# Kernel optimization log

Hardware: AMD Instinct MI355X
Metric: run time of the kernel (lower is better)

Reference implementation:

```python
import jax, jax.numpy as jnp
import numpy as np

LAG = 5
MSG_HID = 256
N_ATOMS = 30
N_EDGES = N_ATOMS * (N_ATOMS - 1)  # 870
BATCH = 2
T = 200


def _rel_matrices():
    # fully-connected directed graph, no self loops (standard NRI encoding)
    recv, send = [], []
    for i in range(N_ATOMS):
        for j in range(N_ATOMS):
            if i != j:
                recv.append(i)
                send.append(j)
    rel_rec = np.zeros((N_EDGES, N_ATOMS), dtype=np.float32)
    rel_send = np.zeros((N_EDGES, N_ATOMS), dtype=np.float32)
    rel_rec[np.arange(N_EDGES), recv] = 1.0
    rel_send[np.arange(N_EDGES), send] = 1.0
    return jnp.asarray(rel_rec), jnp.asarray(rel_send)


def setup_inputs() -> dict:
    key = jax.random.key(0)
    ks = jax.random.split(key, 14)
    rel_rec, rel_send = _rel_matrices()
    s = 0.05
    return {
        "inputs": jax.random.normal(ks[0], (BATCH, N_ATOMS, T), jnp.float32),
        "mu": jax.random.normal(ks[1], (BATCH, N_EDGES), jnp.float32),
        "logvar": jax.random.normal(ks[2], (BATCH, N_EDGES), jnp.float32) * 0.1,
        "eps": jax.random.normal(ks[3], (BATCH, N_EDGES), jnp.float32),
        "rel_rec": rel_rec,
        "rel_send": rel_send,
        "w_msg1": jax.random.normal(ks[4], (2 * LAG, MSG_HID), jnp.float32) * s,
        "b_msg1": jnp.zeros((MSG_HID,), jnp.float32),
        "w_msg2": jax.random.normal(ks[5], (MSG_HID, MSG_HID), jnp.float32) * s,
        "b_msg2": jnp.zeros((MSG_HID,), jnp.float32),
        "w_out1": jax.random.normal(ks[6], (LAG + MSG_HID, MSG_HID), jnp.float32) * s,
        "b_out1": jnp.zeros((MSG_HID,), jnp.float32),
        "w_out2": jax.random.normal(ks[7], (MSG_HID, MSG_HID), jnp.float32) * s,
        "b_out2": jnp.zeros((MSG_HID,), jnp.float32),
        "w_out3": jax.random.normal(ks[8], (MSG_HID, 1), jnp.float32) * s,
        "b_out3": jnp.zeros((1,), jnp.float32),
    }


def reference(inputs, mu, logvar, eps, rel_rec, rel_send,
              w_msg1, b_msg1, w_msg2, b_msg2,
              w_out1, b_out1, w_out2, b_out2, w_out3, b_out3):
    # reparametrize: edges [B, E]
    edges = eps * jnp.exp(0.5 * logvar) + mu

    # lag-stack: data [B, T-lag, N, lag]
    Tm = inputs.shape[2] - LAG
    data = jnp.stack([inputs[:, :, i:i + Tm] for i in range(LAG)], axis=-1)
    data = jnp.transpose(data, (0, 2, 1, 3))  # [B, Tm, N, lag]

    # gather node features to edges via one-hot matmuls
    receivers = jnp.einsum('en,btnl->btel', rel_rec, data)   # [B, Tm, E, lag]
    senders = jnp.einsum('en,btnl->btel', rel_send, data)    # [B, Tm, E, lag]
    pre_msg = jnp.concatenate([senders, receivers], axis=-1)  # [B, Tm, E, 2*lag]

    msg = jax.nn.relu(pre_msg @ w_msg1 + b_msg1)
    msg = jax.nn.relu(msg @ w_msg2 + b_msg2)                 # [B, Tm, E, hid]
    msg = msg * edges[:, None, :, None]                       # edge mask

    # scatter-aggregate messages back to receiver nodes
    agg_msgs = jnp.einsum('bteh,en->btnh', msg, rel_rec)      # [B, Tm, N, hid]

    aug = jnp.concatenate([data, agg_msgs], axis=-1)          # [B, Tm, N, lag+hid]
    pred = jax.nn.relu(aug @ w_out1 + b_out1)
    pred = jax.nn.relu(pred @ w_out2 + b_out2)
    pred = (pred @ w_out3 + b_out3)[..., 0]                   # [B, Tm, N]

    return jnp.transpose(pred, (0, 2, 1))                     # [B, N, Tm]
```

## Files before the change

### kernel.cpp

```cpp
#include <hip/hip_runtime.h>

#define LAG 5
#define HID 256
#define NA 30
#define NE 870
#define TM 195
#define TT 200
#define NB 2
#define EPN 29
#define NTB 98
#define NROWS (NB * TM * NA)
#define APAD 8
#define KC 32
#define UVB 1463
#define W2F_ELEMS (HID * HID)
#define W1F_ELEMS (HID * 288)
#define W2OF_ELEMS (HID * HID)

typedef __bf16 bf16;
typedef __bf16 bf16x8 __attribute__((ext_vector_type(8)));
typedef float floatx4 __attribute__((ext_vector_type(4)));

__global__ __launch_bounds__(256) void k1_prep(
    const float* __restrict__ inputs, const float* __restrict__ w_msg1,
    const float* __restrict__ b_msg1, const float* __restrict__ w_msg2,
    const float* __restrict__ w_out1, const float* __restrict__ w_out2,
    bf16* __restrict__ u, bf16* __restrict__ v, bf16* __restrict__ w2frag,
    bf16* __restrict__ w1frag, bf16* __restrict__ w2ofrag)
{
    const int bid = blockIdx.x, tid = threadIdx.x;
    if (bid < UVB) {
        __shared__ float feats8[8][LAG];
        const int r0 = bid * 8;
        if (tid < 8 * LAG) {
            const int i = tid / LAG, l = tid % LAG;
            const int r = r0 + i;
            float fv = 0.f;
            if (r < NROWS) {
                const int b = r / (TM * NA), rem = r % (TM * NA);
                const int t = rem / NA, n = rem % NA;
                fv = inputs[(b * NA + n) * TT + t + l];
            }
            feats8[i][l] = fv;
        }
        float w1c[2 * LAG];
        #pragma unroll
        for (int k = 0; k < 2 * LAG; ++k) w1c[k] = w_msg1[k * HID + tid];
        const float bb = b_msg1[tid];
        __syncthreads();
        #pragma unroll
        for (int i = 0; i < 8; ++i) {
            const int r = r0 + i;
            if (r < NROWS) {
                float ua = bb, va = 0.f;
                #pragma unroll
                for (int l = 0; l < LAG; ++l) {
                    ua = fmaf(feats8[i][l], w1c[l], ua);
                    va = fmaf(feats8[i][l], w1c[LAG + l], va);
                }
                u[(r << 8) + tid] = (bf16)ua;
                v[(r << 8) + tid] = (bf16)va;
            }
        }
    } else if (bid < UVB + 32) {
        const int fidx = (bid - UVB) * 256 + tid;
        const int lane = fidx & 63;
        const int kc = (fidx >> 6) & 7;
        const int ntc = fidx >> 9;
        const int col = ntc * 16 + (lane & 15);
        const int kb = kc * KC + (lane >> 4) * 8;
        bf16x8 vv;
        #pragma unroll
        for (int x = 0; x < 8; ++x) vv[x] = (bf16)w_msg2[(kb + x) * HID + col];
        *(bf16x8*)&w2frag[fidx * 8] = vv;
    } else if (bid < UVB + 32 + 36) {
        const int fidx = (bid - (UVB + 32)) * 256 + tid;
        const int lane = fidx & 63;
        const int kc = (fidx >> 6) % 9;
        const int ntc = fidx / (64 * 9);
        const int col = ntc * 16 + (lane & 15);
        const int kb = kc * KC + (lane >> 4) * 8;
        bf16x8 vv;
        #pragma unroll
        for (int x = 0; x < 8; ++x) {
            const int k = kb + x;
            float val;
            if (k < 256)      val = w_out1[(5 + k) * HID + col];
            else if (k < 261) val = w_out1[(k - 256) * HID + col];
            else              val = 0.f;
            vv[x] = (bf16)val;
        }
        *(bf16x8*)&w1frag[fidx * 8] = vv;
    } else {
        const int fidx = (bid - (UVB + 32 + 36)) * 256 + tid;
        const int lane = fidx & 63;
        const int kc = (fidx >> 6) & 7;
        const int ntc = fidx >> 9;
        const int col = ntc * 16 + (lane & 15);
        const int kb = kc * KC + (lane >> 4) * 8;
        bf16x8 vv;
        #pragma unroll
        for (int x = 0; x < 8; ++x) vv[x] = (bf16)w_out2[(kb + x) * HID + col];
        *(bf16x8*)&w2ofrag[fidx * 8] = vv;
    }
}

__global__ __launch_bounds__(512) void k2_msg(
    const bf16* __restrict__ u, const bf16* __restrict__ v,
    const bf16* __restrict__ w2frag,
    const float* __restrict__ mu, const float* __restrict__ logvar,
    const float* __restrict__ eps, const float* __restrict__ b_msg2,
    bf16* __restrict__ agg)
{
    __shared__ bf16 a_lds[64][HID + APAD];
    __shared__ float ev_lds[32];

    const int bid = blockIdx.x;
    const int n  = bid % NA;
    const int tb = (bid / NA) % NTB;
    const int b  = bid / (NA * NTB);
    const int t0 = tb * 2;
    const int tid = threadIdx.x;
    const int lane = tid & 63, w = tid >> 6;
    const int q = lane >> 4, m15 = lane & 15;
    const int wbase = w * 32;

    if (tid < 32) {
        float evv = 0.f;
        if (tid < EPN) {
            const int e = b * NE + n * EPN + tid;
            evv = eps[e] * __expf(0.5f * logvar[e]) + mu[e];
        }
        ev_lds[tid] = evv;
    }

    #pragma unroll
    for (int i = 0; i < 4; ++i) {
        const int task = i * 512 + tid;
        const int row = task >> 5, c = task & 31;
        const int tt = row >> 5, ei = row & 31;
        bf16x8 out8;
        if (ei < EPN) {
            int t = t0 + tt; if (t > TM - 1) t = TM - 1;
            const int j = ei + (ei >= n);
            const bf16x8 uu = *(const bf16x8*)(u + ((((b * TM + t) * NA + j) << 8) + c * 8));
            const bf16x8 vv = *(const bf16x8*)(v + ((((b * TM + t) * NA + n) << 8) + c * 8));
            #pragma unroll
            for (int x = 0; x < 8; ++x)
                out8[x] = (bf16)fmaxf((float)uu[x] + (float)vv[x], 0.f);
        } else {
            #pragma unroll
            for (int x = 0; x < 8; ++x) out8[x] = (bf16)0.f;
        }
        *(bf16x8*)&a_lds[row][c * 8] = out8;
    }

    const bf16* bbase = w2frag + (lane << 3);
    bf16x8 bcur[2], bnxt[2];
    #pragma unroll
    for (int nt = 0; nt < 2; ++nt)
        bcur[nt] = *(const bf16x8*)(bbase + (((w * 2 + nt) * 8 + 0) << 9));

    floatx4 acc[4][2];
    #pragma unroll
    for (int mt = 0; mt < 4; ++mt)
        #pragma unroll
        for (int nt = 0; nt < 2; ++nt)
            acc[mt][nt] = (floatx4){0.f, 0.f, 0.f, 0.f};

    __syncthreads();

    #pragma unroll
    for (int kc = 0; kc < 8; ++kc) {
        if (kc < 7) {
            #pragma unroll
            for (int nt = 0; nt < 2; ++nt)
                bnxt[nt] = *(const bf16x8*)(bbase + (((w * 2 + nt) * 8 + kc + 1) << 9));
        }
        bf16x8 af[4];
        #pragma unroll
        for (int mt = 0; mt < 4; ++mt)
            af[mt] = *(const bf16x8*)&a_lds[mt * 16 + m15][kc * KC + q * 8];
        #pragma unroll
        for (int nt = 0; nt < 2; ++nt)
            #pragma unroll
            for (int mt = 0; mt < 4; ++mt)
                acc[mt][nt] = __builtin_amdgcn_mfma_f32_16x16x32_bf16(af[mt], bcur[nt], acc[mt][nt], 0, 0, 0);
        #pragma unroll
        for (int nt = 0; nt < 2; ++nt) bcur[nt] = bnxt[nt];
    }

    float b2v[2];
    #pragma unroll
    for (int nt = 0; nt < 2; ++nt) b2v[nt] = b_msg2[wbase + nt * 16 + m15];

    #pragma unroll
    for (int tt = 0; tt < 2; ++tt) {
        const int t = t0 + tt;
        #pragma unroll
        for (int nt = 0; nt < 2; ++nt) {
            float part = 0.f;
            #pragma unroll
            for (int ml = 0; ml < 2; ++ml) {
                const int mt = tt * 2 + ml;
                #pragma unroll
                for (int reg = 0; reg < 4; ++reg) {
                    const int ei = (ml * 16 + q * 4 + reg);
                    part += ev_lds[ei] * fmaxf(acc[mt][nt][reg] + b2v[nt], 0.f);
                }
            }
            part += __shfl_xor(part, 16, 64);
            part += __shfl_xor(part, 32, 64);
            if (q == 0 && t < TM)
                agg[((((b * TM + t) * NA + n) << 8) + wbase + nt * 16 + m15)] = (bf16)part;
        }
    }
}

__global__ __launch_bounds__(256) void k3_out(
    const bf16* __restrict__ agg, const float* __restrict__ inputs,
    const bf16* __restrict__ w1frag, const bf16* __restrict__ w2ofrag,
    const float* __restrict__ b_out1, const float* __restrict__ b_out2,
    const float* __restrict__ w_out3, const float* __restrict__ b_out3,
    float* __restrict__ out)
{
    __shared__ bf16 a1[16][288 + APAD];
    __shared__ float red[4][16];

    const int R0 = blockIdx.x * 16;
    const int tid = threadIdx.x;
    const int lane = tid & 63, w = tid >> 6;
    const int q = lane >> 4, m15 = lane & 15;
    const int wbase = w * 64;

    #pragma unroll
    for (int i = 0; i < 2; ++i) {
        const int task = i * 256 + tid;
        const int row = task >> 5, c = task & 31;
        const int R = R0 + row;
        bf16x8 val;
        if (R < NROWS) {
            val = *(const bf16x8*)&agg[(R << 8) + c * 8];
        } else {
            for (int x = 0; x < 8; ++x) val[x] = (bf16)0.f;
        }
        *(bf16x8*)&a1[row][c * 8] = val;
    }
    if (tid < 16) {
        const int R = R0 + tid;
        if (R < NROWS) {
            const int b = R / (TM * NA), rem = R % (TM * NA);
            const int t = rem / NA, n = rem % NA;
            const float* ip = inputs + (b * NA + n) * TT + t;
            #pragma unroll
            for (int l = 0; l < LAG; ++l) a1[tid][256 + l] = (bf16)ip[l];
            #pragma unroll
            for (int k = 261; k < 288; ++k) a1[tid][k] = (bf16)0.f;
        } else {
            for (int k = 256; k < 288; ++k) a1[tid][k] = (bf16)0.f;
        }
    }

    floatx4 acc[4];
    #pragma unroll
    for (int nt = 0; nt < 4; ++nt) acc[nt] = (floatx4){0.f, 0.f, 0.f, 0.f};

    const bf16* b1base = w1frag + (lane << 3);
    bf16x8 bcur[4], bnxt[4];
    #pragma unroll
    for (int nt = 0; nt < 4; ++nt)
        bcur[nt] = *(const bf16x8*)(b1base + (((w * 4 + nt) * 9 + 0) << 9));

    __syncthreads();

    #pragma unroll
    for (int kc = 0; kc < 9; ++kc) {
        if (kc < 8) {
            #pragma unroll
            for (int nt = 0; nt < 4; ++nt)
                bnxt[nt] = *(const bf16x8*)(b1base + (((w * 4 + nt) * 9 + kc + 1) << 9));
        }
        const bf16x8 af = *(const bf16x8*)&a1[m15][kc * KC + q * 8];
        #pragma unroll
        for (int nt = 0; nt < 4; ++nt)
            acc[nt] = __builtin_amdgcn_mfma_f32_16x16x32_bf16(af, bcur[nt], acc[nt], 0, 0, 0);
        #pragma unroll
        for (int nt = 0; nt < 4; ++nt) bcur[nt] = bnxt[nt];
    }
    __syncthreads();

    {
        float b1v[4];
        #pragma unroll
        for (int nt = 0; nt < 4; ++nt) b1v[nt] = b_out1[wbase + nt * 16 + m15];
        #pragma unroll
        for (int nt = 0; nt < 4; ++nt)
            #pragma unroll
            for (int reg = 0; reg < 4; ++reg)
                a1[q * 4 + reg][wbase + nt * 16 + m15] =
                    (bf16)fmaxf(acc[nt][reg] + b1v[nt], 0.f);
    }

    #pragma unroll
    for (int nt = 0; nt < 4; ++nt) acc[nt] = (floatx4){0.f, 0.f, 0.f, 0.f};

    const bf16* b2base = w2ofrag + (lane << 3);
    #pragma unroll
    for (int nt = 0; nt < 4; ++nt)
        bcur[nt] = *(const bf16x8*)(b2base + (((w * 4 + nt) * 8 + 0) << 9));

    __syncthreads();

    #pragma unroll
    for (int kc = 0; kc < 8; ++kc) {
        if (kc < 7) {
            #pragma unroll
            for (int nt = 0; nt < 4; ++nt)
                bnxt[nt] = *(const bf16x8*)(b2base + (((w * 4 + nt) * 8 + kc + 1) << 9));
        }
        const bf16x8 af = *(const bf16x8*)&a1[m15][kc * KC + q * 8];
        #pragma unroll
        for (int nt = 0; nt < 4; ++nt)
            acc[nt] = __builtin_amdgcn_mfma_f32_16x16x32_bf16(af, bcur[nt], acc[nt], 0, 0, 0);
        #pragma unroll
        for (int nt = 0; nt < 4; ++nt) bcur[nt] = bnxt[nt];
    }

    {
        float b2v[4], w3v[4];
        #pragma unroll
        for (int nt = 0; nt < 4; ++nt) {
            const int col = wbase + nt * 16 + m15;
            b2v[nt] = b_out2[col];
            w3v[nt] = w_out3[col];
        }
        #pragma unroll
        for (int reg = 0; reg < 4; ++reg) {
            float p = 0.f;
            #pragma unroll
            for (int nt = 0; nt < 4; ++nt)
                p += fmaxf(acc[nt][reg] + b2v[nt], 0.f) * w3v[nt];
            p += __shfl_xor(p, 1, 64);
            p += __shfl_xor(p, 2, 64);
            p += __shfl_xor(p, 4, 64);
            p += __shfl_xor(p, 8, 64);
            if (m15 == 0) red[w][q * 4 + reg] = p;
        }
    }
    __syncthreads();
    if (tid < 16) {
        const int R = R0 + tid;
        if (R < NROWS) {
            const float val = red[0][tid] + red[1][tid] + red[2][tid] + red[3][tid] + b_out3[0];
            const int b = R / (TM * NA), rem = R % (TM * NA);
            const int t = rem / NA, n = rem % NA;
            out[(b * NA + n) * TM + t] = val;
        }
    }
}

extern "C" void kernel_launch(void* const* d_in, const int* in_sizes, int n_in,
                              void* d_out, int out_size, void* d_ws, size_t ws_size,
                              hipStream_t stream) {
    const float* inputs  = (const float*)d_in[0];
    const float* mu      = (const float*)d_in[1];
    const float* logvar  = (const float*)d_in[2];
    const float* eps     = (const float*)d_in[3];
    const float* w_msg1  = (const float*)d_in[6];
    const float* b_msg1  = (const float*)d_in[7];
    const float* w_msg2  = (const float*)d_in[8];
    const float* b_msg2  = (const float*)d_in[9];
    const float* w_out1  = (const float*)d_in[10];
    const float* b_out1  = (const float*)d_in[11];
    const float* w_out2  = (const float*)d_in[12];
    const float* b_out2  = (const float*)d_in[13];
    const float* w_out3  = (const float*)d_in[14];
    const float* b_out3  = (const float*)d_in[15];
    float* out = (float*)d_out;

    bf16* u       = (bf16*)d_ws;
    bf16* v       = u       + NROWS * HID;
    bf16* aggw    = v       + NROWS * HID;
    bf16* w2frag  = aggw    + NROWS * HID;
    bf16* w1frag  = w2frag  + W2F_ELEMS;
    bf16* w2ofrag = w1frag  + W1F_ELEMS;

    hipLaunchKernelGGL(k1_prep, dim3(UVB + 32 + 36 + 32), dim3(256), 0, stream,
                       inputs, w_msg1, b_msg1, w_msg2, w_out1, w_out2,
                       u, v, w2frag, w1frag, w2ofrag);
    hipLaunchKernelGGL(k2_msg, dim3(NB * NA * NTB), dim3(512), 0, stream,
                       u, v, w2frag, mu, logvar, eps, b_msg2, aggw);
    hipLaunchKernelGGL(k3_out, dim3((NROWS + 15) / 16), dim3(256), 0, stream,
                       aggw, inputs, w1frag, w2ofrag, b_out1, b_out2, w_out3, b_out3, out);
}
```

Before: 168.8 us.

## Switch to fp16 MFMA, process three timesteps per message block, deepen weight prefetch

Changes all intermediate activations and weight fragments from bf16 to fp16 and uses the f16 MFMA instruction. The ReLU of u+v becomes a packed half-precision add and max instead of per-element float conversions. The message kernel now covers three timesteps per block (96 rows), so each B fragment is reused across more M tiles and the tail clamp goes away because 195 divides by 3. It also prefetches weights two K-chunks ahead, sets a min-blocks-per-SM launch bound and shrinks LDS padding. fp16 has less exponent range than bf16, a no-op term was added in w2ofrag prep, and the larger tile raises register and LDS use, which may lower occupancy.

```diff
diff --git a/kernel.cpp b/kernel.cpp
--- a/kernel.cpp
+++ b/kernel.cpp
@@ -8,25 +8,24 @@
 #define TT 200
 #define NB 2
 #define EPN 29
-#define NTB 98
+#define TB3 65
 #define NROWS (NB * TM * NA)
-#define APAD 8
+#define APAD 4
 #define KC 32
 #define UVB 1463
 #define W2F_ELEMS (HID * HID)
 #define W1F_ELEMS (HID * 288)
-#define W2OF_ELEMS (HID * HID)
-
-typedef __bf16 bf16;
-typedef __bf16 bf16x8 __attribute__((ext_vector_type(8)));
+
+typedef _Float16 f16;
+typedef _Float16 f16x8 __attribute__((ext_vector_type(8)));
 typedef float floatx4 __attribute__((ext_vector_type(4)));
 
 __global__ __launch_bounds__(256) void k1_prep(
     const float* __restrict__ inputs, const float* __restrict__ w_msg1,
     const float* __restrict__ b_msg1, const float* __restrict__ w_msg2,
     const float* __restrict__ w_out1, const float* __restrict__ w_out2,
-    bf16* __restrict__ u, bf16* __restrict__ v, bf16* __restrict__ w2frag,
-    bf16* __restrict__ w1frag, bf16* __restrict__ w2ofrag)
+    f16* __restrict__ u, f16* __restrict__ v, f16* __restrict__ w2frag,
+    f16* __restrict__ w1frag, f16* __restrict__ w2ofrag)
 {
     const int bid = blockIdx.x, tid = threadIdx.x;
     if (bid < UVB) {
@@ -58,8 +57,8 @@
                     ua = fmaf(feats8[i][l], w1c[l], ua);
                     va = fmaf(feats8[i][l], w1c[LAG + l], va);
                 }
-                u[(r << 8) + tid] = (bf16)ua;
-                v[(r << 8) + tid] = (bf16)va;
+                u[(r << 8) + tid] = (f16)ua;
+                v[(r << 8) + tid] = (f16)va;
             }
         }
     } else if (bid < UVB + 32) {
@@ -69,10 +68,10 @@
         const int ntc = fidx >> 9;
         const int col = ntc * 16 + (lane & 15);
         const int kb = kc * KC + (lane >> 4) * 8;
-        bf16x8 vv;
-        #pragma unroll
-        for (int x = 0; x < 8; ++x) vv[x] = (bf16)w_msg2[(kb + x) * HID + col];
-        *(bf16x8*)&w2frag[fidx * 8] = vv;
+        f16x8 vv;
+        #pragma unroll
+        for (int x = 0; x < 8; ++x) vv[x] = (f16)w_msg2[(kb + x) * HID + col];
+        *(f16x8*)&w2frag[fidx * 8] = vv;
     } else if (bid < UVB + 32 + 36) {
         const int fidx = (bid - (UVB + 32)) * 256 + tid;
         const int lane = fidx & 63;
@@ -80,7 +79,7 @@
         const int ntc = fidx / (64 * 9);
         const int col = ntc * 16 + (lane & 15);
         const int kb = kc * KC + (lane >> 4) * 8;
-        bf16x8 vv;
+        f16x8 vv;
         #pragma unroll
         for (int x = 0; x < 8; ++x) {
             const int k = kb + x;
@@ -88,9 +87,9 @@
             if (k < 256)      val = w_out1[(5 + k) * HID + col];
             else if (k < 261) val = w_out1[(k - 256) * HID + col];
             else              val = 0.f;
-            vv[x] = (bf16)val;
-        }
-        *(bf16x8*)&w1frag[fidx * 8] = vv;
+            vv[x] = (f16)val;
+        }
+        *(f16x8*)&w1frag[fidx * 8] = vv;
     } else {
         const int fidx = (bid - (UVB + 32 + 36)) * 256 + tid;
         const int lane = fidx & 63;
@@ -98,28 +97,28 @@
         const int ntc = fidx >> 9;
         const int col = ntc * 16 + (lane & 15);
         const int kb = kc * KC + (lane >> 4) * 8;
-        bf16x8 vv;
-        #pragma unroll
-        for (int x = 0; x < 8; ++x) vv[x] = (bf16)w_out2[(kb + x) * HID + col];
-        *(bf16x8*)&w2ofrag[fidx * 8] = vv;
+        f16x8 vv;
+        #pragma unroll
+        for (int x = 0; x < 8; ++x) vv[x] = (f16)w_msg2[0] * (f16)0.f + (f16)w_out2[(kb + x) * HID + col];
+        *(f16x8*)&w2ofrag[fidx * 8] = vv;
     }
 }
 
-__global__ __launch_bounds__(512) void k2_msg(
-    const bf16* __restrict__ u, const bf16* __restrict__ v,
-    const bf16* __restrict__ w2frag,
+__global__ __launch_bounds__(512, 4) void k2_msg(
+    const f16* __restrict__ u, const f16* __restrict__ v,
+    const f16* __restrict__ w2frag,
     const float* __restrict__ mu, const float* __restrict__ logvar,
     const float* __restrict__ eps, const float* __restrict__ b_msg2,
-    bf16* __restrict__ agg)
+    f16* __restrict__ agg)
 {
-    __shared__ bf16 a_lds[64][HID + APAD];
+    __shared__ f16 a_lds[96][HID + APAD];
     __shared__ float ev_lds[32];
 
     const int bid = blockIdx.x;
     const int n  = bid % NA;
-    const int tb = (bid / NA) % NTB;
-    const int b  = bid / (NA * NTB);
-    const int t0 = tb * 2;
+    const int tb = (bid / NA) % TB3;
+    const int b  = bid / (NA * TB3);
+    const int t0 = tb * 3;
     const int tid = threadIdx.x;
     const int lane = tid & 63, w = tid >> 6;
     const int q = lane >> 4, m15 = lane & 15;
@@ -134,36 +133,37 @@
         ev_lds[tid] = evv;
     }
 
-    #pragma unroll
-    for (int i = 0; i < 4; ++i) {
+    const f16x8 z8 = {(f16)0, (f16)0, (f16)0, (f16)0, (f16)0, (f16)0, (f16)0, (f16)0};
+
+    #pragma unroll
+    for (int i = 0; i < 6; ++i) {
         const int task = i * 512 + tid;
         const int row = task >> 5, c = task & 31;
         const int tt = row >> 5, ei = row & 31;
-        bf16x8 out8;
+        f16x8 out8;
         if (ei < EPN) {
-            int t = t0 + tt; if (t > TM - 1) t = TM - 1;
+            const int t = t0 + tt;
             const int j = ei + (ei >= n);
-            const bf16x8 uu = *(const bf16x8*)(u + ((((b * TM + t) * NA + j) << 8) + c * 8));
-            const bf16x8 vv = *(const bf16x8*)(v + ((((b * TM + t) * NA + n) << 8) + c * 8));
-            #pragma unroll
-            for (int x = 0; x < 8; ++x)
-                out8[x] = (bf16)fmaxf((float)uu[x] + (float)vv[x], 0.f);
+            const f16x8 uu = *(const f16x8*)(u + ((((b * TM + t) * NA + j) << 8) + c * 8));
+            const f16x8 vv = *(const f16x8*)(v + ((((b * TM + t) * NA + n) << 8) + c * 8));
+            out8 = __builtin_elementwise_max(uu + vv, z8);
         } else {
-            #pragma unroll
-            for (int x = 0; x < 8; ++x) out8[x] = (bf16)0.f;
-        }
-        *(bf16x8*)&a_lds[row][c * 8] = out8;
-    }
-
-    const bf16* bbase = w2frag + (lane << 3);
-    bf16x8 bcur[2], bnxt[2];
-    #pragma unroll
-    for (int nt = 0; nt < 2; ++nt)
-        bcur[nt] = *(const bf16x8*)(bbase + (((w * 2 + nt) * 8 + 0) << 9));
-
-    floatx4 acc[4][2];
-    #pragma unroll
-    for (int mt = 0; mt < 4; ++mt)
+            out8 = z8;
+        }
+        *(f16x8*)&a_lds[row][c * 8] = out8;
+    }
+
+    const f16* bbase = w2frag + (lane << 3);
+    f16x8 b0[2], b1[2], b2[2];
+    #pragma unroll
+    for (int nt = 0; nt < 2; ++nt) {
+        b0[nt] = *(const f16x8*)(bbase + (((w * 2 + nt) * 8 + 0) << 9));
+        b1[nt] = *(const f16x8*)(bbase + (((w * 2 + nt) * 8 + 1) << 9));
+    }
+
+    floatx4 acc[6][2];
+    #pragma unroll
+    for (int mt = 0; mt < 6; ++mt)
         #pragma unroll
         for (int nt = 0; nt < 2; ++nt)
             acc[mt][nt] = (floatx4){0.f, 0.f, 0.f, 0.f};
@@ -172,22 +172,22 @@
 
     #pragma unroll
     for (int kc = 0; kc < 8; ++kc) {
-        if (kc < 7) {
+        if (kc < 6) {
             #pragma unroll
             for (int nt = 0; nt < 2; ++nt)
-                bnxt[nt] = *(const bf16x8*)(bbase + (((w * 2 + nt) * 8 + kc + 1) << 9));
-        }
-        bf16x8 af[4];
-        #pragma unroll
-        for (int mt = 0; mt < 4; ++mt)
-            af[mt] = *(const bf16x8*)&a_lds[mt * 16 + m15][kc * KC + q * 8];
+                b2[nt] = *(const f16x8*)(bbase + (((w * 2 + nt) * 8 + kc + 2) << 9));
+        }
+        f16x8 af[6];
+        #pragma unroll
+        for (int mt = 0; mt < 6; ++mt)
+            af[mt] = *(const f16x8*)&a_lds[mt * 16 + m15][kc * KC + q * 8];
         #pragma unroll
         for (int nt = 0; nt < 2; ++nt)
             #pragma unroll
-            for (int mt = 0; mt < 4; ++mt)
-                acc[mt][nt] = __builtin_amdgcn_mfma_f32_16x16x32_bf16(af[mt], bcur[nt], acc[mt][nt], 0, 0, 0);
-        #pragma unroll
-        for (int nt = 0; nt < 2; ++nt) bcur[nt] = bnxt[nt];
+            for (int mt = 0; mt < 6; ++mt)
+                acc[mt][nt] = __builtin_amdgcn_mfma_f32_16x16x32_f16(af[mt], b0[nt], acc[mt][nt], 0, 0, 0);
+        #pragma unroll
+        for (int nt = 0; nt < 2; ++nt) { b0[nt] = b1[nt]; b1[nt] = b2[nt]; }
     }
 
     float b2v[2];
@@ -195,7 +195,7 @@
     for (int nt = 0; nt < 2; ++nt) b2v[nt] = b_msg2[wbase + nt * 16 + m15];
 
     #pragma unroll
-    for (int tt = 0; tt < 2; ++tt) {
+    for (int tt = 0; tt < 3; ++tt) {
         const int t = t0 + tt;
         #pragma unroll
         for (int nt = 0; nt < 2; ++nt) {
@@ -211,20 +211,20 @@
             }
             part += __shfl_xor(part, 16, 64);
             part += __shfl_xor(part, 32, 64);
-            if (q == 0 && t < TM)
-                agg[((((b * TM + t) * NA + n) << 8) + wbase + nt * 16 + m15)] = (bf16)part;
+            if (q == 0)
+                agg[((((b * TM + t) * NA + n) << 8) + wbase + nt * 16 + m15)] = (f16)part;
         }
     }
 }
 
 __global__ __launch_bounds__(256) void k3_out(
-    const bf16* __restrict__ agg, const float* __restrict__ inputs,
-    const bf16* __restrict__ w1frag, const bf16* __restrict__ w2ofrag,
+    const f16* __restrict__ agg, const float* __restrict__ inputs,
+    const f16* __restrict__ w1frag, const f16* __restrict__ w2ofrag,
     const float* __restrict__ b_out1, const float* __restrict__ b_out2,
     const float* __restrict__ w_out3, const float* __restrict__ b_out3,
     float* __restrict__ out)
 {
-    __shared__ bf16 a1[16][288 + APAD];
+    __shared__ f16 a1[16][288 + APAD];
     __shared__ float red[4][16];
 
     const int R0 = blockIdx.x * 16;
@@ -238,13 +238,13 @@
         const int task = i * 256 + tid;
         const int row = task >> 5, c = task & 31;
         const int R = R0 + row;
-        bf16x8 val;
+        f16x8 val;
         if (R < NROWS) {
-            val = *(const bf16x8*)&agg[(R << 8) + c * 8];
+            val = *(const f16x8*)&agg[(R << 8) + c * 8];
         } else {
-            for (int x = 0; x < 8; ++x) val[x] = (bf16)0.f;
-        }
-        *(bf16x8*)&a1[row][c * 8] = val;
+            for (int x = 0; x < 8; ++x) val[x] = (f16)0.f;
+        }
+        *(f16x8*)&a1[row][c * 8] = val;
     }
     if (tid < 16) {
         const int R = R0 + tid;
@@ -253,11 +253,11 @@
             const int t = rem / NA, n = rem % NA;
             const float* ip = inputs + (b * NA + n) * TT + t;
             #pragma unroll
-            for (int l = 0; l < LAG; ++l) a1[tid][256 + l] = (bf16)ip[l];
-            #pragma unroll
-            for (int k = 261; k < 288; ++k) a1[tid][k] = (bf16)0.f;
+            for (int l = 0; l < LAG; ++l) a1[tid][256 + l] = (f16)ip[l];
+            #pragma unroll
+            for (int k = 261; k < 288; ++k) a1[tid][k] = (f16)0.f;
         } else {
-            for (int k = 256; k < 288; ++k) a1[tid][k] = (bf16)0.f;
+            for (int k = 256; k < 288; ++k) a1[tid][k] = (f16)0.f;
         }
     }
 
@@ -265,11 +265,11 @@
     #pragma unroll
     for (int nt = 0; nt < 4; ++nt) acc[nt] = (floatx4){0.f, 0.f, 0.f, 0.f};
 
-    const bf16* b1base = w1frag + (lane << 3);
-    bf16x8 bcur[4], bnxt[4];
+    const f16* b1base = w1frag + (lane << 3);
+    f16x8 bcur[4], bnxt[4];
     #pragma unroll
     for (int nt = 0; nt < 4; ++nt)
-        bcur[nt] = *(const bf16x8*)(b1base + (((w * 4 + nt) * 9 + 0) << 9));
+        bcur[nt] = *(const f16x8*)(b1base + (((w * 4 + nt) * 9 + 0) << 9));
 
     __syncthreads();
 
@@ -278,12 +278,12 @@
         if (kc < 8) {
             #pragma unroll
             for (int nt = 0; nt < 4; ++nt)
-                bnxt[nt] = *(const bf16x8*)(b1base + (((w * 4 + nt) * 9 + kc + 1) << 9));
-        }
-        const bf16x8 af = *(const bf16x8*)&a1[m15][kc * KC + q * 8];
+                bnxt[nt] = *(const f16x8*)(b1base + (((w * 4 + nt) * 9 + kc + 1) << 9));
+        }
+        const f16x8 af = *(const f16x8*)&a1[m15][kc * KC + q * 8];
         #pragma unroll
         for (int nt = 0; nt < 4; ++nt)
-            acc[nt] = __builtin_amdgcn_mfma_f32_16x16x32_bf16(af, bcur[nt], acc[nt], 0, 0, 0);
+            acc[nt] = __builtin_amdgcn_mfma_f32_16x16x32_f16(af, bcur[nt], acc[nt], 0, 0, 0);
         #pragma unroll
         for (int nt = 0; nt < 4; ++nt) bcur[nt] = bnxt[nt];
     }
@@ -298,16 +298,16 @@
             #pragma unroll
             for (int reg = 0; reg < 4; ++reg)
                 a1[q * 4 + reg][wbase + nt * 16 + m15] =
-                    (bf16)fmaxf(acc[nt][reg] + b1v[nt], 0.f);
+                    (f16)fmaxf(acc[nt][reg] + b1v[nt], 0.f);
     }
 
     #pragma unroll
     for (int nt = 0; nt < 4; ++nt) acc[nt] = (floatx4){0.f, 0.f, 0.f, 0.f};
 
-    const bf16* b2base = w2ofrag + (lane << 3);
+    const f16* b2base = w2ofrag + (lane << 3);
     #pragma unroll
     for (int nt = 0; nt < 4; ++nt)
-        bcur[nt] = *(const bf16x8*)(b2base + (((w * 4 + nt) * 8 + 0) << 9));
+        bcur[nt] = *(const f16x8*)(b2base + (((w * 4 + nt) * 8 + 0) << 9));
 
     __syncthreads();
 
@@ -316,12 +316,12 @@
         if (kc < 7) {
             #pragma unroll
             for (int nt = 0; nt < 4; ++nt)
-                bnxt[nt] = *(const bf16x8*)(b2base + (((w * 4 + nt) * 8 + kc + 1) << 9));
-        }
-        const bf16x8 af = *(const bf16x8*)&a1[m15][kc * KC + q * 8];
+                bnxt[nt] = *(const f16x8*)(b2base + (((w * 4 + nt) * 8 + kc + 1) << 9));
+        }
+        const f16x8 af = *(const f16x8*)&a1[m15][kc * KC + q * 8];
         #pragma unroll
         for (int nt = 0; nt < 4; ++nt)
-            acc[nt] = __builtin_amdgcn_mfma_f32_16x16x32_bf16(af, bcur[nt], acc[nt], 0, 0, 0);
+            acc[nt] = __builtin_amdgcn_mfma_f32_16x16x32_f16(af, bcur[nt], acc[nt], 0, 0, 0);
         #pragma unroll
         for (int nt = 0; nt < 4; ++nt) bcur[nt] = bnxt[nt];
     }
@@ -378,17 +378,17 @@
     const float* b_out3  = (const float*)d_in[15];
     float* out = (float*)d_out;
 
-    bf16* u       = (bf16*)d_ws;
-    bf16* v       = u       + NROWS * HID;
-    bf16* aggw    = v       + NROWS * HID;
-    bf16* w2frag  = aggw    + NROWS * HID;
-    bf16* w1frag  = w2frag  + W2F_ELEMS;
-    bf16* w2ofrag = w1frag  + W1F_ELEMS;
+    f16* u       = (f16*)d_ws;
+    f16* v       = u       + NROWS * HID;
+    f16* aggw    = v       + NROWS * HID;
+    f16* w2frag  = aggw    + NROWS * HID;
+    f16* w1frag  = w2frag  + W2F_ELEMS;
+    f16* w2ofrag = w1frag  + W1F_ELEMS;
 
     hipLaunchKernelGGL(k1_prep, dim3(UVB + 32 + 36 + 32), dim3(256), 0, stream,
                        inputs, w_msg1, b_msg1, w_msg2, w_out1, w_out2,
                        u, v, w2frag, w1frag, w2ofrag);
-    hipLaunchKernelGGL(k2_msg, dim3(NB * NA * NTB), dim3(512), 0, stream,
+    hipLaunchKernelGGL(k2_msg, dim3(NB * NA * TB3), dim3(512), 0, stream,
                        u, v, w2frag, mu, logvar, eps, b_msg2, aggw);
     hipLaunchKernelGGL(k3_out, dim3((NROWS + 15) / 16), dim3(256), 0, stream,
                        aggw, inputs, w1frag, w2ofrag, b_out1, b_out2, w_out3, b_out3, out);
```

Result: faster. 156.5 us (-7.3%).
